# Performance work log

Hardware: AMD Instinct MI355X
Metric: run time of the kernel (lower is better)

## Reference

```python
import math
import jax, jax.numpy as jnp
import numpy as np

B, S, D = 4, 2048, 1024
H, HD = 16, 64
NUM_BUCKETS = 32
MAX_DISTANCE = 128
EPS = 1e-6
ENC_S = 512


def _relative_position_bucket(relative_position):
    # bidirectional=False path
    num_buckets = NUM_BUCKETS
    rp = -jnp.minimum(relative_position, 0)  # [S, S] nonneg
    max_exact = num_buckets // 2
    is_small = rp < max_exact
    scale = (num_buckets - max_exact) / math.log(MAX_DISTANCE / max_exact)
    large = max_exact + (jnp.log(jnp.maximum(rp, 1).astype(jnp.float32) / max_exact) * scale).astype(jnp.int32)
    large = jnp.minimum(large, num_buckets - 1)
    return jnp.where(is_small, rp, large)


def compute_bias(rel_emb, q_len, k_len):
    ctx = jnp.arange(q_len)[:, None]
    mem = jnp.arange(k_len)[None, :]
    bucket = _relative_position_bucket(mem - ctx)          # [q, k] int
    values = rel_emb[bucket]                                # [q, k, H]
    return jnp.transpose(values, (2, 0, 1))[None]           # [1, H, q, k]


def setup_inputs() -> dict:
    key = jax.random.key(0)
    ks = jax.random.split(key, 8)
    std = 0.02
    return {
        "input_ids": jax.random.normal(ks[0], (B, S, D), jnp.float32),
        "encoder_output": jax.random.normal(ks[1], (B, ENC_S, D), jnp.float32),
        "wq": jax.random.normal(ks[2], (D, H * HD), jnp.float32) * std,
        "wk": jax.random.normal(ks[3], (D, H * HD), jnp.float32) * std,
        "wv": jax.random.normal(ks[4], (D, H * HD), jnp.float32) * std,
        "wo": jax.random.normal(ks[5], (H * HD, D), jnp.float32) * std,
        "rel_emb": jax.random.normal(ks[6], (NUM_BUCKETS, H), jnp.float32) * std,
        "ln_w": jnp.ones((D,), jnp.float32),
    }


def reference(input_ids, encoder_output, wq, wk, wv, wo, rel_emb, ln_w):
    origin = input_ids
    # MT5LayerNorm: RMS norm, no mean subtraction, no bias
    variance = jnp.mean(jnp.square(input_ids.astype(jnp.float32)), axis=-1, keepdims=True)
    x = (input_ids * jax.lax.rsqrt(variance + EPS)) * ln_w

    q = (x @ wq).reshape(B, S, H, HD)
    k = (x @ wk).reshape(B, S, H, HD)
    v = (x @ wv).reshape(B, S, H, HD)

    # NOTE: T5-style attention has no 1/sqrt(d) scaling
    scores = jnp.einsum("bqhd,bkhd->bhqk", q, k)
    scores = scores + compute_bias(rel_emb, S, S)
    attn = jax.nn.softmax(scores, axis=-1)
    ctx = jnp.einsum("bhqk,bkhd->bqhd", attn, v).reshape(B, S, H * HD)
    attn_out = ctx @ wo

    # residual connection (dropout is identity at rate 0 / eval)
    return origin + attn_out
```

## Files before the change

### kernel.cpp

```cpp
#include <hip/hip_runtime.h>
#include <hip/hip_bf16.h>
#include <math.h>

#define S_LEN 2048
#define D_DIM 1024
#define NHEAD 16

typedef __attribute__((ext_vector_type(8))) short bf16x8;
typedef __attribute__((ext_vector_type(4))) float floatx4;

__device__ __forceinline__ short f32_bf16(float f) {
  union { float f; unsigned u; } v; v.f = f;
  unsigned r = v.u + 0x7FFFu + ((v.u >> 16) & 1u);
  return (short)(r >> 16);
}

__device__ __forceinline__ float exp2_fast(float x) {
#if __has_builtin(__builtin_amdgcn_exp2f)
  return __builtin_amdgcn_exp2f(x);
#else
  float r; asm("v_exp_f32 %0, %1" : "=v"(r) : "v"(x)); return r;
#endif
}

__device__ __forceinline__ void gload16(const void* g, void* l) {
  __builtin_amdgcn_global_load_lds((const __attribute__((address_space(1))) unsigned*)g,
                                   (__attribute__((address_space(3))) unsigned*)l,
                                   16, 0, 0);
}

__global__ __launch_bounds__(256) void prep_k(const float* __restrict__ x,
                                              const float* __restrict__ lnw,
                                              const float* __restrict__ wq,
                                              const float* __restrict__ wk,
                                              const float* __restrict__ wv,
                                              const float* __restrict__ wo,
                                              short* __restrict__ xb,
                                              short* __restrict__ oqkv,
                                              short* __restrict__ owo) {
  if (blockIdx.x < 8192) {
    int row = blockIdx.x;
    const float4* xr = (const float4*)(x + (size_t)row * D_DIM);
    float4 v = xr[threadIdx.x];
    float ss = v.x*v.x + v.y*v.y + v.z*v.z + v.w*v.w;
    #pragma unroll
    for (int off = 32; off > 0; off >>= 1) ss += __shfl_xor(ss, off);
    __shared__ float red[4];
    if ((threadIdx.x & 63) == 0) red[threadIdx.x >> 6] = ss;
    __syncthreads();
    float scale = rsqrtf((red[0]+red[1]+red[2]+red[3]) * (1.f/D_DIM) + 1e-6f);
    float4 wv4 = ((const float4*)lnw)[threadIdx.x];
    short4 o;
    o.x = f32_bf16(v.x*scale*wv4.x);
    o.y = f32_bf16(v.y*scale*wv4.y);
    o.z = f32_bf16(v.z*scale*wv4.z);
    o.w = f32_bf16(v.w*scale*wv4.w);
    ((short4*)xb)[(size_t)row*256 + threadIdx.x] = o;
  } else {
    __shared__ float tile[64][65];
    int id = blockIdx.x - 8192;
    int m  = id >> 8;
    int tt = id & 255;
    int tn = tt >> 4, tk = tt & 15;
    const float* src = (m == 0) ? wq : (m == 1) ? wk : (m == 2) ? wv : wo;
    float scale = (m == 0) ? 1.44269504f : 1.0f;
    int t = threadIdx.x;
    int kl  = t >> 4;
    int nl4 = t & 15;
    #pragma unroll
    for (int i = 0; i < 4; i++) {
      int k = i*16 + kl;
      float4 v = *(const float4*)&src[(size_t)(tk*64 + k)*1024 + tn*64 + nl4*4];
      tile[k][nl4*4+0] = v.x;
      tile[k][nl4*4+1] = v.y;
      tile[k][nl4*4+2] = v.z;
      tile[k][nl4*4+3] = v.w;
    }
    __syncthreads();
    short* dst = (m < 3) ? oqkv : owo;
    size_t nbase = (m < 3) ? (size_t)m * 1024 : 0;
    #pragma unroll
    for (int i = 0; i < 2; i++) {
      int idx = i*256 + t;
      int nl = idx >> 3;
      int g  = idx & 7;
      short tmp[8];
      #pragma unroll
      for (int j = 0; j < 8; j++) tmp[j] = f32_bf16(tile[g*8 + j][nl] * scale);
      *(bf16x8*)&dst[(nbase + tn*64 + nl)*1024 + tk*64 + g*8] = *(bf16x8*)tmp;
    }
  }
}

template<bool WRITE_VT, bool ADD_RES>
__global__ __launch_bounds__(512) void gemm256(const short* __restrict__ A,
                                               const short* __restrict__ Bt,
                                               short* __restrict__ Cb,
                                               float* __restrict__ Cf,
                                               const float* __restrict__ res,
                                               short* __restrict__ vt,
                                               int N, int NBN) {
  __shared__ __align__(16) short As[4][256*32];
  __shared__ __align__(16) short Bs[4][128*32];
  const int tid = threadIdx.x;
  const int w = tid >> 6, lane = tid & 63, quad = lane >> 4, l16 = lane & 15;
  const int wm = w >> 2, wn = w & 3;
  const int id = blockIdx.x;
  const int o = (id & 7) * (gridDim.x >> 3) + (id >> 3);
  const int bm = o / NBN, bn = o % NBN;
  const short* Ag = A  + (size_t)bm * 256 * 1024;
  const short* Bg = Bt + (size_t)bn * 128 * 1024;
  const int r4 = lane >> 2, c4 = lane & 3;
  const int lc  = c4 ^ ((r4 >> 1) & 3);
  const int swz = (quad ^ ((l16 >> 1) & 3)) * 8;

  floatx4 acc[8][2] = {};

  #define SA(t_) do {                                                          \
    gload16(Ag + (size_t)((w    )*16 + r4) * 1024 + (t_)*32 + lc*8,            \
            &As[(t_) & 3][(w    )*512]);                                       \
    gload16(Ag + (size_t)((w + 8)*16 + r4) * 1024 + (t_)*32 + lc*8,            \
            &As[(t_) & 3][(w + 8)*512]);                                       \
  } while (0)
  #define SB(t_) do {                                                          \
    gload16(Bg + (size_t)((w    )*16 + r4) * 1024 + (t_)*32 + lc*8,            \
            &Bs[(t_) & 3][(w    )*512]);                                       \
  } while (0)

  #define PH(t_, STG_, VMW_) do {                                              \
    const short* Ab = &As[(t_) & 3][0];                                        \
    const short* Bb = &Bs[(t_) & 3][0];                                        \
    bf16x8 af[8], bf0, bf1;                                                    \
    _Pragma("unroll")                                                          \
    for (int i = 0; i < 8; i++)                                                \
      af[i] = *(const bf16x8*)&Ab[(wm*128 + i*16 + l16)*32 + swz];             \
    bf0 = *(const bf16x8*)&Bb[(wn*32 +  0 + l16)*32 + swz];                    \
    if (STG_) SA((t_) + 3);                                                    \
    asm volatile("s_waitcnt lgkmcnt(0)");                                      \
    __builtin_amdgcn_sched_barrier(0);                                         \
    __builtin_amdgcn_s_setprio(1);                                             \
    _Pragma("unroll")                                                          \
    for (int i = 0; i < 8; i++)                                                \
      acc[i][0] = __builtin_amdgcn_mfma_f32_16x16x32_bf16(af[i], bf0, acc[i][0], 0, 0, 0); \
    __builtin_amdgcn_s_setprio(0);                                             \
    bf1 = *(const bf16x8*)&Bb[(wn*32 + 16 + l16)*32 + swz];                    \
    if (STG_) SB((t_) + 3);                                                    \
    asm volatile("s_waitcnt lgkmcnt(0)");                                      \
    __builtin_amdgcn_sched_barrier(0);                                         \
    __builtin_amdgcn_s_setprio(1);                                             \
    _Pragma("unroll")                                                          \
    for (int i = 0; i < 8; i++)                                                \
      acc[i][1] = __builtin_amdgcn_mfma_f32_16x16x32_bf16(af[i], bf1, acc[i][1], 0, 0, 0); \
    __builtin_amdgcn_s_setprio(0);                                             \
    asm volatile("s_waitcnt " VMW_);                                           \
    __builtin_amdgcn_s_barrier();                                              \
    __builtin_amdgcn_sched_barrier(0);                                         \
  } while (0)

  SA(0); SB(0); SA(1); SB(1); SA(2); SB(2);
  asm volatile("s_waitcnt vmcnt(6)");
  __builtin_amdgcn_s_barrier();
  __builtin_amdgcn_sched_barrier(0);

  #pragma unroll 1
  for (int t = 0; t < 29; ++t) PH(t, true, "vmcnt(6)");
  PH(29, false, "vmcnt(3)");
  PH(30, false, "vmcnt(0)");
  PH(31, false, "vmcnt(0)");
  #undef SA
  #undef SB
  #undef PH

  if (WRITE_VT && bn >= 16) {
    #pragma unroll
    for (int i = 0; i < 8; i++) {
      int row0 = bm*256 + wm*128 + i*16 + quad*4;
      int b = row0 >> 11, s = row0 & 2047;
      #pragma unroll
      for (int j = 0; j < 2; j++) {
        int hcol = (bn - 16)*128 + wn*32 + j*16 + l16;
        short4 st;
        st.x = f32_bf16(acc[i][j][0]);
        st.y = f32_bf16(acc[i][j][1]);
        st.z = f32_bf16(acc[i][j][2]);
        st.w = f32_bf16(acc[i][j][3]);
        int bh = (b << 4) + (hcol >> 6);
        *(short4*)&vt[((size_t)(bh*64 + (hcol & 63)))*2048 + s] = st;
      }
    }
    return;
  }

  #pragma unroll
  for (int i = 0; i < 8; i++) {
    int row0 = bm*256 + wm*128 + i*16 + quad*4;
    #pragma unroll
    for (int j = 0; j < 2; j++) {
      int col = bn*128 + wn*32 + j*16 + l16;
      #pragma unroll
      for (int r = 0; r < 4; r++) {
        size_t idx = (size_t)(row0 + r) * N + col;
        if (ADD_RES) Cf[idx] = res[idx] + acc[i][j][r];
        else         Cb[idx] = f32_bf16(acc[i][j][r]);
      }
    }
  }
}

__global__ __launch_bounds__(512) void flash_k(const short* __restrict__ qkv,
                                               const short* __restrict__ vt,
                                               const float* __restrict__ rel_emb,
                                               short* __restrict__ ctx) {
  __shared__ __align__(16) short Kb[2][64*64];
  __shared__ __align__(16) short Vb[3][64*64];
  __shared__ float lut2[132];

  const int L = blockIdx.x + 8*blockIdx.y;
  const int xcd = L & 7, kk_ = L >> 3;
  const int bh = xcd*8 + (kk_ >> 3);
  const int qt = kk_ & 7;
  const int b = bh >> 4, h = bh & 15;
  const int t = threadIdx.x, w = t >> 6, lane = t & 63, quad = lane >> 4, l16 = lane & 15;
  const float L2E = 1.44269504f;

  if (t < 129) {
    int rp = t, bucket;
    if (rp < 16) bucket = rp;
    else {
      bucket = 16 + (int)(logf((float)rp * 0.0625f) * (16.f / logf(8.f)));
      if (bucket > 31) bucket = 31;
    }
    lut2[t] = rel_emb[bucket*16 + h] * L2E;
  }
  const float bfut  = rel_emb[h] * L2E;
  const float bpast = rel_emb[31*16 + h] * L2E;
  const floatx4 bf4 = {bfut, bfut, bfut, bfut};
  const floatx4 bp4 = {bpast, bpast, bpast, bpast};
  const floatx4 zz4 = {0.f, 0.f, 0.f, 0.f};

  const int srow = lane >> 3;
  const int slc  = (lane & 7) ^ srow;
  const int rho  = w*8 + srow;
  const int kperm = 32*(rho >> 5) + 8*((rho >> 2) & 3) + 4*((rho >> 4) & 1) + (rho & 3);

  const short* kgU = qkv + ((size_t)b*S_LEN)*3072 + 1024 + h*64;
  const int    loK = kperm*3072 + slc*8;
  const short* vgU = vt + ((size_t)bh*64)*2048;
  const int    loV = rho*2048 + slc*8;

  {
    bf16x8 z = {};
    *(bf16x8*)&Vb[2][t*8] = z;
  }

  bf16x8 qB[2][2];
  #pragma unroll
  for (int rb = 0; rb < 2; rb++) {
    const short* qb = qkv + ((size_t)(b*S_LEN + qt*256 + rb*128 + w*16 + l16))*3072 + h*64;
    qB[rb][0] = *(const bf16x8*)&qb[quad*8];
    qB[rb][1] = *(const bf16x8*)&qb[32 + quad*8];
  }

  floatx4 o[2][4] = {};
  floatx4 li4[2] = {};
  const short ONE = (short)0x3F80;
  bf16x8 onesA = {ONE, ONE, ONE, ONE, ONE, ONE, ONE, ONE};
  bf16x8 pfP[2][2] = {};

  const int swz0 = (quad     ^ (l16 & 7)) * 8;
  const int swz1 = ((quad+4) ^ (l16 & 7)) * 8;

  int vnext = 1;
  int vprev = 2;

  #define STAGE_T(KP_, VN_, KT_) do {                                           \
    const short* ka_ = kgU + (size_t)(KT_)*196608 + loK;                        \
    gload16(ka_, &Kb[KP_][(w*8)*64]);                                           \
    const short* va_ = vgU + loV + (KT_)*64;                                    \
    gload16(va_, &Vb[VN_][(w*8)*64]);                                           \
  } while (0)

  #define BODY(P_, KT_) do {                                                    \
    __syncthreads();                                                            \
    if ((KT_) < 31) STAGE_T((P_) ^ 1, vnext, (KT_) + 1);                        \
    bool boundary = ((KT_) >= 4*qt - 2) && ((KT_) <= 4*qt + 3);                 \
    floatx4 cinit = boundary ? zz4 : (((KT_) >= 4*qt) ? bf4 : bp4);             \
    floatx4 sc[2][4];                                                           \
    _Pragma("unroll")                                                           \
    for (int c = 0; c < 4; c++) {                                               \
      int rowA = (c*16 + l16)*64;                                               \
      bf16x8 ka0 = *(const bf16x8*)&Kb[P_][rowA + swz0];                        \
      bf16x8 ka1 = *(const bf16x8*)&Kb[P_][rowA + swz1];                        \
      _Pragma("unroll")                                                         \
      for (int rb = 0; rb < 2; rb++) {                                          \
        floatx4 z = __builtin_amdgcn_mfma_f32_16x16x32_bf16(ka0, qB[rb][0], cinit, 0, 0, 0); \
        z = __builtin_amdgcn_mfma_f32_16x16x32_bf16(ka1, qB[rb][1], z, 0, 0, 0);\
        sc[rb][c] = z;                                                          \
      }                                                                         \
    }                                                                           \
    if (boundary) {                                                             \
      _Pragma("unroll")                                                         \
      for (int rb = 0; rb < 2; rb++) {                                          \
        int q0 = qt*256 + rb*128 + w*16 + l16;                                  \
        _Pragma("unroll")                                                       \
        for (int c = 0; c < 4; c++) {                                           \
          int kk = (KT_)*64 + 32*(c >> 1) + 8*quad + 4*(c & 1);                 \
          _Pragma("unroll")                                                     \
          for (int r = 0; r < 4; r++) {                                         \
            int d = q0 - (kk + r);                                              \
            d = d < 0 ? 0 : (d > 128 ? 128 : d);                                \
            sc[rb][c][r] += lut2[d];                                            \
          }                                                                     \
        }                                                                       \
      }                                                                         \
    }                                                                           \
    _Pragma("unroll")                                                           \
    for (int rb = 0; rb < 2; rb++)                                              \
      _Pragma("unroll")                                                         \
      for (int c = 0; c < 4; c++)                                               \
        _Pragma("unroll")                                                       \
        for (int r = 0; r < 4; r++)                                             \
          sc[rb][c][r] = exp2_fast(sc[rb][c][r]);                               \
    bf16x8 pfL[2][2];                                                           \
    _Pragma("unroll")                                                           \
    for (int rb = 0; rb < 2; rb++) {                                            \
      _Pragma("unroll")                                                         \
      for (int hh = 0; hh < 2; hh++) {                                          \
        union { bf16x8 v; unsigned u[4]; } pk;                                  \
        floatx4 a = sc[rb][2*hh], bb = sc[rb][2*hh + 1];                        \
        pk.u[0] = __builtin_amdgcn_perm(__float_as_uint(a[1]),  __float_as_uint(a[0]),  0x07060302); \
        pk.u[1] = __builtin_amdgcn_perm(__float_as_uint(a[3]),  __float_as_uint(a[2]),  0x07060302); \
        pk.u[2] = __builtin_amdgcn_perm(__float_as_uint(bb[1]), __float_as_uint(bb[0]), 0x07060302); \
        pk.u[3] = __builtin_amdgcn_perm(__float_as_uint(bb[3]), __float_as_uint(bb[2]), 0x07060302); \
        pfL[rb][hh] = pk.v;                                                     \
      }                                                                         \
    }                                                                           \
                 \
    _Pragma("unroll")                                                           \
    for (int jj = 0; jj < 4; jj++) {                                            \
      int rowV = (jj*16 + l16)*64;                                              \
      bf16x8 va0 = *(const bf16x8*)&Vb[vprev][rowV + swz0];                     \
      bf16x8 va1 = *(const bf16x8*)&Vb[vprev][rowV + swz1];                     \
      _Pragma("unroll")                                                         \
      for (int rb = 0; rb < 2; rb++) {                                          \
        o[rb][jj] = __builtin_amdgcn_mfma_f32_16x16x32_bf16(va0, pfP[rb][0], o[rb][jj], 0, 0, 0); \
        o[rb][jj] = __builtin_amdgcn_mfma_f32_16x16x32_bf16(va1, pfP[rb][1], o[rb][jj], 0, 0, 0); \
      }                                                                         \
    }                                                                           \
    _Pragma("unroll")                                                           \
    for (int rb = 0; rb < 2; rb++) {                                            \
      li4[rb] = __builtin_amdgcn_mfma_f32_16x16x32_bf16(onesA, pfL[rb][0], li4[rb], 0, 0, 0); \
      li4[rb] = __builtin_amdgcn_mfma_f32_16x16x32_bf16(onesA, pfL[rb][1], li4[rb], 0, 0, 0); \
    }                                                                           \
    _Pragma("unroll")                                                           \
    for (int rb = 0; rb < 2; rb++) {                                            \
      pfP[rb][0] = pfL[rb][0];                                                  \
      pfP[rb][1] = pfL[rb][1];                                                  \
    }                                                                           \
    vprev = (vprev == 2) ? 0 : vprev + 1;                                       \
    vnext = (vnext == 2) ? 0 : vnext + 1;                                       \
  } while (0)

  STAGE_T(0, 0, 0);
  for (int kt = 0; kt < 32; kt += 2) {
    BODY(0, kt);
    BODY(1, kt + 1);
  }

  #pragma unroll
  for (int jj = 0; jj < 4; jj++) {
    int rowV = (jj*16 + l16)*64;
    bf16x8 va0 = *(const bf16x8*)&Vb[vprev][rowV + swz0];
    bf16x8 va1 = *(const bf16x8*)&Vb[vprev][rowV + swz1];
    #pragma unroll
    for (int rb = 0; rb < 2; rb++) {
      o[rb][jj] = __builtin_amdgcn_mfma_f32_16x16x32_bf16(va0, pfP[rb][0], o[rb][jj], 0, 0, 0);
      o[rb][jj] = __builtin_amdgcn_mfma_f32_16x16x32_bf16(va1, pfP[rb][1], o[rb][jj], 0, 0, 0);
    }
  }

  #pragma unroll
  for (int rb = 0; rb < 2; rb++) {
    float inv = 1.f / li4[rb][0];
    size_t row = (size_t)(b*S_LEN + qt*256 + rb*128 + w*16 + l16);
    #pragma unroll
    for (int jj = 0; jj < 4; jj++) {
      short4 st;
      st.x = f32_bf16(o[rb][jj][0] * inv);
      st.y = f32_bf16(o[rb][jj][1] * inv);
      st.z = f32_bf16(o[rb][jj][2] * inv);
      st.w = f32_bf16(o[rb][jj][3] * inv);
      *(short4*)&ctx[row*1024 + h*64 + jj*16 + quad*4] = st;
    }
  }
  #undef STAGE_T
  #undef BODY
}

extern "C" void kernel_launch(void* const* d_in, const int* in_sizes, int n_in,
                              void* d_out, int out_size, void* d_ws, size_t ws_size,
                              hipStream_t stream) {
  const float* input_ids = (const float*)d_in[0];
  const float* wq      = (const float*)d_in[2];
  const float* wk      = (const float*)d_in[3];
  const float* wv      = (const float*)d_in[4];
  const float* wo      = (const float*)d_in[5];
  const float* rel_emb = (const float*)d_in[6];
  const float* ln_w    = (const float*)d_in[7];
  float* out = (float*)d_out;

  char* ws = (char*)d_ws;
  short* xb     = (short*)ws;  ws += (size_t)8192*1024*2;
  short* wqkv_t = (short*)ws;  ws += (size_t)3072*1024*2;
  short* wo_t   = (short*)ws;  ws += (size_t)1024*1024*2;
  short* qkv    = (short*)ws;  ws += (size_t)8192*3072*2;
  short* vt     = (short*)ws;  ws += (size_t)64*64*2048*2;
  short* ctx    = (short*)ws;  ws += (size_t)8192*1024*2;

  prep_k<<<8192 + 1024, 256, 0, stream>>>(input_ids, ln_w, wq, wk, wv, wo,
                                          xb, wqkv_t, wo_t);
  gemm256<true, false><<<768, 512, 0, stream>>>(xb, wqkv_t, qkv, nullptr,
                                                nullptr, vt, 3072, 24);
  flash_k<<<dim3(8, 64), 512, 0, stream>>>(qkv, vt, rel_emb, ctx);
  gemm256<false, true><<<256, 512, 0, stream>>>(ctx, wo_t, nullptr, out,
                                                input_ids, nullptr, 1024, 8);
}
```

Before: 288.3 us.

## Remove deferred PV software pipelining in flash attention kernel

Result: faster. 269.1 us (-6.7%).

```diff
diff --git a/kernel.cpp b/kernel.cpp
--- a/kernel.cpp
+++ b/kernel.cpp
@@ -212,7 +212,7 @@
                                                const float* __restrict__ rel_emb,
                                                short* __restrict__ ctx) {
   __shared__ __align__(16) short Kb[2][64*64];
-  __shared__ __align__(16) short Vb[3][64*64];
+  __shared__ __align__(16) short Vb[2][64*64];
   __shared__ float lut2[132];
 
   const int L = blockIdx.x + 8*blockIdx.y;
@@ -248,11 +248,6 @@
   const short* vgU = vt + ((size_t)bh*64)*2048;
   const int    loV = rho*2048 + slc*8;
 
-  {
-    bf16x8 z = {};
-    *(bf16x8*)&Vb[2][t*8] = z;
-  }
-
   bf16x8 qB[2][2];
   #pragma unroll
   for (int rb = 0; rb < 2; rb++) {
@@ -265,24 +260,20 @@
   floatx4 li4[2] = {};
   const short ONE = (short)0x3F80;
   bf16x8 onesA = {ONE, ONE, ONE, ONE, ONE, ONE, ONE, ONE};
-  bf16x8 pfP[2][2] = {};
 
   const int swz0 = (quad     ^ (l16 & 7)) * 8;
   const int swz1 = ((quad+4) ^ (l16 & 7)) * 8;
 
-  int vnext = 1;
-  int vprev = 2;
-
-  #define STAGE_T(KP_, VN_, KT_) do {                                           \
+  #define STAGE(P_, KT_) do {                                                   \
     const short* ka_ = kgU + (size_t)(KT_)*196608 + loK;                        \
-    gload16(ka_, &Kb[KP_][(w*8)*64]);                                           \
+    gload16(ka_, &Kb[P_][(w*8)*64]);                                            \
     const short* va_ = vgU + loV + (KT_)*64;                                    \
-    gload16(va_, &Vb[VN_][(w*8)*64]);                                           \
+    gload16(va_, &Vb[P_][(w*8)*64]);                                            \
   } while (0)
 
   #define BODY(P_, KT_) do {                                                    \
     __syncthreads();                                                            \
-    if ((KT_) < 31) STAGE_T((P_) ^ 1, vnext, (KT_) + 1);                        \
+    if ((KT_) < 31) STAGE((P_) ^ 1, (KT_) + 1);                                 \
     bool boundary = ((KT_) >= 4*qt - 2) && ((KT_) <= 4*qt + 3);                 \
     floatx4 cinit = boundary ? zz4 : (((KT_) >= 4*qt) ? bf4 : bp4);             \
     floatx4 sc[2][4];                                                           \
@@ -321,7 +312,7 @@
         _Pragma("unroll")                                                       \
         for (int r = 0; r < 4; r++)                                             \
           sc[rb][c][r] = exp2_fast(sc[rb][c][r]);                               \
-    bf16x8 pfL[2][2];                                                           \
+    bf16x8 pf[2][2];                                                            \
     _Pragma("unroll")                                                           \
     for (int rb = 0; rb < 2; rb++) {                                            \
       _Pragma("unroll")                                                         \
@@ -332,51 +323,31 @@
         pk.u[1] = __builtin_amdgcn_perm(__float_as_uint(a[3]),  __float_as_uint(a[2]),  0x07060302); \
         pk.u[2] = __builtin_amdgcn_perm(__float_as_uint(bb[1]), __float_as_uint(bb[0]), 0x07060302); \
         pk.u[3] = __builtin_amdgcn_perm(__float_as_uint(bb[3]), __float_as_uint(bb[2]), 0x07060302); \
-        pfL[rb][hh] = pk.v;                                                     \
+        pf[rb][hh] = pk.v;                                                      \
       }                                                                         \
     }                                                                           \
-                 \
+    _Pragma("unroll")                                                           \
+    for (int rb = 0; rb < 2; rb++) {                                            \
+      li4[rb] = __builtin_amdgcn_mfma_f32_16x16x32_bf16(onesA, pf[rb][0], li4[rb], 0, 0, 0); \
+      li4[rb] = __builtin_amdgcn_mfma_f32_16x16x32_bf16(onesA, pf[rb][1], li4[rb], 0, 0, 0); \
+    }                                                                           \
     _Pragma("unroll")                                                           \
     for (int jj = 0; jj < 4; jj++) {                                            \
       int rowV = (jj*16 + l16)*64;                                              \
-      bf16x8 va0 = *(const bf16x8*)&Vb[vprev][rowV + swz0];                     \
-      bf16x8 va1 = *(const bf16x8*)&Vb[vprev][rowV + swz1];                     \
+      bf16x8 va0 = *(const bf16x8*)&Vb[P_][rowV + swz0];                        \
+      bf16x8 va1 = *(const bf16x8*)&Vb[P_][rowV + swz1];                        \
       _Pragma("unroll")                                                         \
       for (int rb = 0; rb < 2; rb++) {                                          \
-        o[rb][jj] = __builtin_amdgcn_mfma_f32_16x16x32_bf16(va0, pfP[rb][0], o[rb][jj], 0, 0, 0); \
-        o[rb][jj] = __builtin_amdgcn_mfma_f32_16x16x32_bf16(va1, pfP[rb][1], o[rb][jj], 0, 0, 0); \
+        o[rb][jj] = __builtin_amdgcn_mfma_f32_16x16x32_bf16(va0, pf[rb][0], o[rb][jj], 0, 0, 0); \
+        o[rb][jj] = __builtin_amdgcn_mfma_f32_16x16x32_bf16(va1, pf[rb][1], o[rb][jj], 0, 0, 0); \
       }                                                                         \
     }                                                                           \
-    _Pragma("unroll")                                                           \
-    for (int rb = 0; rb < 2; rb++) {                                            \
-      li4[rb] = __builtin_amdgcn_mfma_f32_16x16x32_bf16(onesA, pfL[rb][0], li4[rb], 0, 0, 0); \
-      li4[rb] = __builtin_amdgcn_mfma_f32_16x16x32_bf16(onesA, pfL[rb][1], li4[rb], 0, 0, 0); \
-    }                                                                           \
-    _Pragma("unroll")                                                           \
-    for (int rb = 0; rb < 2; rb++) {                                            \
-      pfP[rb][0] = pfL[rb][0];                                                  \
-      pfP[rb][1] = pfL[rb][1];                                                  \
-    }                                                                           \
-    vprev = (vprev == 2) ? 0 : vprev + 1;                                       \
-    vnext = (vnext == 2) ? 0 : vnext + 1;                                       \
-  } while (0)
-
-  STAGE_T(0, 0, 0);
+  } while (0)
+
+  STAGE(0, 0);
   for (int kt = 0; kt < 32; kt += 2) {
     BODY(0, kt);
     BODY(1, kt + 1);
-  }
-
-  #pragma unroll
-  for (int jj = 0; jj < 4; jj++) {
-    int rowV = (jj*16 + l16)*64;
-    bf16x8 va0 = *(const bf16x8*)&Vb[vprev][rowV + swz0];
-    bf16x8 va1 = *(const bf16x8*)&Vb[vprev][rowV + swz1];
-    #pragma unroll
-    for (int rb = 0; rb < 2; rb++) {
-      o[rb][jj] = __builtin_amdgcn_mfma_f32_16x16x32_bf16(va0, pfP[rb][0], o[rb][jj], 0, 0, 0);
-      o[rb][jj] = __builtin_amdgcn_mfma_f32_16x16x32_bf16(va1, pfP[rb][1], o[rb][jj], 0, 0, 0);
-    }
   }
 
   #pragma unroll
@@ -393,7 +364,7 @@
       *(short4*)&ctx[row*1024 + h*64 + jj*16 + quad*4] = st;
     }
   }
-  #undef STAGE_T
+  #undef STAGE
   #undef BODY
 }
 
```
